# Performance work log

Measured on AMD Instinct MI355X. Metric: run time of the kernel, lower is better.

The kernel has to match this reference:

```python
import jax, jax.numpy as jnp
import numpy as np

N_HEADS = 4
N_GROUPS = 32
EPS = 1e-5


def setup_inputs() -> dict:
    key = jax.random.key(0)
    ks = jax.random.split(key, 6)
    c = 512
    x = jax.random.normal(ks[0], (4, c, 64, 64), dtype=jnp.float32)
    # conv1x1 weights ~ kaiming-ish scale
    s = 1.0 / np.sqrt(c)
    wq = jax.random.normal(ks[1], (c, c), dtype=jnp.float32) * s
    wk = jax.random.normal(ks[2], (c, c), dtype=jnp.float32) * s
    wv = jax.random.normal(ks[3], (c, c), dtype=jnp.float32) * s
    wp = jax.random.normal(ks[4], (c, c), dtype=jnp.float32) * s
    zeros = jnp.zeros((c,), dtype=jnp.float32)
    return {
        "x": x,
        "gn_w": jnp.ones((c,), dtype=jnp.float32), "gn_b": zeros,
        "wq": wq, "bq": zeros, "wk": wk, "bk": zeros,
        "wv": wv, "bv": zeros, "wp": wp, "bp": zeros,
    }


def _group_norm(x, w, b):
    bsz, c, h, wd = x.shape
    xg = x.reshape(bsz, N_GROUPS, c // N_GROUPS, h, wd)
    mean = xg.mean(axis=(2, 3, 4), keepdims=True)
    var = xg.var(axis=(2, 3, 4), keepdims=True)
    xg = (xg - mean) * jax.lax.rsqrt(var + EPS)
    x = xg.reshape(bsz, c, h, wd)
    return x * w[None, :, None, None] + b[None, :, None, None]


def _conv1x1(x, w, b):
    # x: (b,c,h,w), w: (out,in) -> (b,out,h,w)
    return jnp.einsum('bchw,oc->bohw', x, w) + b[None, :, None, None]


def reference(x, gn_w, gn_b, wq, bq, wk, bk, wv, bv, wp, bp):
    bsz, c, h, wd = x.shape
    hd = c // N_HEADS
    hw = h * wd
    x_n = _group_norm(x, gn_w, gn_b)
    q = _conv1x1(x_n, wq, bq)
    k = _conv1x1(x_n, wk, bk)
    v = _conv1x1(x_n, wv, bv)

    def to_heads(t):
        # (b,c,h,w) -> (b, n_heads, hw, head_dim)
        return t.reshape(bsz, N_HEADS, hd, hw).transpose(0, 1, 3, 2)

    q, k, v = to_heads(q), to_heads(k), to_heads(v)
    scale = hd ** (-0.5)
    attn = jnp.einsum('bhqd,bhkd->bhqk', q, k) * scale  # (b,H,hw,hw)
    attn = jax.nn.softmax(attn, axis=-1)
    out = jnp.einsum('bhqk,bhkd->bhqd', attn, v)
    out = out.transpose(0, 1, 3, 2).reshape(bsz, c, h, wd)
    out = _conv1x1(out, wp, bp)
    return x + out
```

## Files before the change

kernel.cpp:

```cpp
#include <hip/hip_runtime.h>
#include <math.h>

typedef __attribute__((ext_vector_type(8))) short short8;
typedef __attribute__((ext_vector_type(4))) float floatx4;
typedef __attribute__((ext_vector_type(16))) float floatx16;
typedef __attribute__((ext_vector_type(8))) unsigned short ushort8v;
typedef __attribute__((ext_vector_type(4))) unsigned short ushort4v;

#define HW 4096
#define CCH 512
#define NB 4
#define NH 4
#define HD 128

__device__ __forceinline__ unsigned short f2bf(float f) {
    union { float f; unsigned int u; } c; c.f = f;
    unsigned int u = c.u;
    u += 0x7FFFu + ((u >> 16) & 1u);
    return (unsigned short)(u >> 16);
}

__device__ __forceinline__ void gload_lds16(const unsigned short* g, unsigned short* l) {
    __builtin_amdgcn_global_load_lds(
        (const __attribute__((address_space(1))) unsigned int*)g,
        (__attribute__((address_space(3))) unsigned int*)l, 16, 0, 0);
}

__global__ void conv_w(const float* __restrict__ w0, const float* __restrict__ w1,
                       const float* __restrict__ w2, const float* __restrict__ w3,
                       unsigned short* __restrict__ dst) {
    const float* src = blockIdx.y == 0 ? w0 : blockIdx.y == 1 ? w1 : blockIdx.y == 2 ? w2 : w3;
    unsigned short* d = dst + (size_t)blockIdx.y * 262144;
    int i = blockIdx.x * 256 + threadIdx.x;
    float4 v = ((const float4*)src)[i];
    ushort4v o;
    o[0] = f2bf(v.x); o[1] = f2bf(v.y); o[2] = f2bf(v.z); o[3] = f2bf(v.w);
    ((ushort4v*)d)[i] = o;
}

__global__ void gn_stats(const float* __restrict__ x, float* __restrict__ stats) {
    int bg = blockIdx.x;
    int b = bg >> 5, g = bg & 31;
    const float4* p = (const float4*)(x + ((size_t)b * CCH + g * 16) * HW);
    float s = 0.f, ss = 0.f;
    for (int i = threadIdx.x; i < 16384; i += 256) {
        float4 v = p[i];
        s  += v.x + v.y + v.z + v.w;
        ss += v.x * v.x + v.y * v.y + v.z * v.z + v.w * v.w;
    }
    #pragma unroll
    for (int off = 32; off > 0; off >>= 1) {
        s  += __shfl_down(s, off, 64);
        ss += __shfl_down(ss, off, 64);
    }
    __shared__ float sm[4], sm2[4];
    int wid = threadIdx.x >> 6;
    if ((threadIdx.x & 63) == 0) { sm[wid] = s; sm2[wid] = ss; }
    __syncthreads();
    if (threadIdx.x == 0) {
        float ts = sm[0] + sm[1] + sm[2] + sm[3];
        float tss = sm2[0] + sm2[1] + sm2[2] + sm2[3];
        float mean = ts * (1.f / 65536.f);
        float var = tss * (1.f / 65536.f) - mean * mean;
        stats[bg * 2] = mean;
        stats[bg * 2 + 1] = rsqrtf(var + 1e-5f);
    }
}

__global__ void gn_apply(const float* __restrict__ x, const float* __restrict__ gnw,
                         const float* __restrict__ gnb, const float* __restrict__ stats,
                         unsigned short* __restrict__ xt) {
    int s = blockIdx.x * 256 + threadIdx.x;
    int g = blockIdx.y, b = blockIdx.z;
    float mean = stats[(b * 32 + g) * 2];
    float rstd = stats[(b * 32 + g) * 2 + 1];
    const float* xb = x + ((size_t)b * CCH + g * 16) * HW + s;
    unsigned short outv[16];
    #pragma unroll
    for (int cl = 0; cl < 16; cl++) {
        int c = g * 16 + cl;
        float v = xb[(size_t)cl * HW];
        v = (v - mean) * rstd * gnw[c] + gnb[c];
        outv[cl] = f2bf(v);
    }
    unsigned short* dst = xt + ((size_t)b * HW + s) * CCH + g * 16;
    *(ushort8v*)dst       = *(ushort8v*)&outv[0];
    *(ushort8v*)(dst + 8) = *(ushort8v*)&outv[8];
}

template <int MODE>
__global__ __launch_bounds__(256, 3) void gemm_nt(
    const unsigned short* __restrict__ A, long long aStride,
    const unsigned short* __restrict__ Bm, long long bStride,
    const float* __restrict__ bias, float scale,
    const float* __restrict__ resid, long long rStride,
    void* __restrict__ Cp, long long cStride, int ldc) {
    __shared__ __align__(16) unsigned short lA[128 * 64];
    __shared__ __align__(16) unsigned short lB[128 * 64];
    const int tid = threadIdx.x;
    const int lane = tid & 63;
    const int wid = tid >> 6;
    const int z = blockIdx.z;
    const unsigned short* Ab = A + (size_t)z * aStride + (size_t)blockIdx.x * 128 * 512;
    const unsigned short* Bb = Bm + (size_t)z * bStride + (size_t)blockIdx.y * 128 * 512;

    floatx4 acc[4][4];
    #pragma unroll
    for (int i = 0; i < 4; i++)
        #pragma unroll
        for (int j = 0; j < 4; j++) acc[i][j] = (floatx4)0.f;

    const int wm = (wid >> 1) * 64;
    const int wn = (wid & 1) * 64;
    const int l15 = lane & 15;
    const int l4 = lane >> 4;
    const int sxr = l15 & 7;

    size_t srcOff[4];
    int dstBase[4];
    #pragma unroll
    for (int n = 0; n < 4; n++) {
        int row = n * 32 + (tid >> 3);
        int g = tid & 7;
        srcOff[n] = (size_t)row * 512 + (size_t)((g ^ (row & 7)) << 3);
        dstBase[n] = (n * 256 + wid * 64) * 8;
    }

    #pragma unroll 1
    for (int t = 0; t < 8; t++) {
        int k0 = t * 64;
        #pragma unroll
        for (int n = 0; n < 4; n++) gload_lds16(&Ab[srcOff[n] + k0], lA + dstBase[n]);
        #pragma unroll
        for (int n = 0; n < 4; n++) gload_lds16(&Bb[srcOff[n] + k0], lB + dstBase[n]);
        __syncthreads();
        #pragma unroll
        for (int kk = 0; kk < 2; kk++) {
            short8 af[4], bf[4];
            #pragma unroll
            for (int i = 0; i < 4; i++)
                af[i] = *(const short8*)&lA[(wm + i * 16 + l15) * 64 + (((kk * 4 + l4) ^ sxr) << 3)];
            #pragma unroll
            for (int j = 0; j < 4; j++)
                bf[j] = *(const short8*)&lB[(wn + j * 16 + l15) * 64 + (((kk * 4 + l4) ^ sxr) << 3)];
            #pragma unroll
            for (int i = 0; i < 4; i++)
                #pragma unroll
                for (int j = 0; j < 4; j++)
                    acc[i][j] = __builtin_amdgcn_mfma_f32_16x16x32_bf16(af[i], bf[j], acc[i][j], 0, 0, 0);
        }
        if (t < 7) __syncthreads();
    }

    long long m0 = (long long)blockIdx.x * 128 + wm;
    long long n0 = (long long)blockIdx.y * 128 + wn;
    if (MODE == 3 && blockIdx.z == 1) {
        unsigned short* C = (unsigned short*)Cp + (size_t)cStride;
        #pragma unroll
        for (int i = 0; i < 4; i++)
            #pragma unroll
            for (int j = 0; j < 4; j++) {
                long long col = n0 + j * 16 + l15;
                float bv = resid[col];
                int hh = (int)(col >> 7);
                int d = (int)(col & 127);
                size_t dpart = (size_t)(d >> 3) * 512 + (size_t)(d & 7);
                #pragma unroll
                for (int r = 0; r < 4; r++) {
                    long long row = m0 + i * 16 + l4 * 4 + r;
                    int bb = (int)(row >> 12), s = (int)(row & 4095);
                    size_t addr = (size_t)(bb * NH + hh) * 524288
                                + (size_t)(s >> 6) * 8192 + dpart + (size_t)(s & 63) * 8;
                    C[addr] = f2bf(acc[i][j][r] + bv);
                }
            }
    } else if (MODE == 0 || MODE == 3) {
        unsigned short* C = (unsigned short*)Cp + (size_t)z * cStride;
        #pragma unroll
        for (int i = 0; i < 4; i++)
            #pragma unroll
            for (int j = 0; j < 4; j++) {
                long long col = n0 + j * 16 + l15;
                float bv = bias[col];
                #pragma unroll
                for (int r = 0; r < 4; r++) {
                    long long row = m0 + i * 16 + l4 * 4 + r;
                    C[row * ldc + col] = f2bf((acc[i][j][r] + bv) * scale);
                }
            }
    } else if (MODE == 1) {
        float* C = (float*)Cp + (size_t)z * cStride;
        const float* R = resid + (size_t)z * rStride;
        #pragma unroll
        for (int i = 0; i < 4; i++)
            #pragma unroll
            for (int j = 0; j < 4; j++)
                #pragma unroll
                for (int r = 0; r < 4; r++) {
                    long long row = m0 + i * 16 + l4 * 4 + r;
                    long long col = n0 + j * 16 + l15;
                    C[row * ldc + col] = acc[i][j][r] + bias[row] + R[row * ldc + col];
                }
    } else {
        unsigned short* C = (unsigned short*)Cp;
        const int b = z;
        #pragma unroll
        for (int i = 0; i < 4; i++)
            #pragma unroll
            for (int j = 0; j < 4; j++)
                #pragma unroll
                for (int r = 0; r < 4; r++) {
                    long long row = m0 + i * 16 + l4 * 4 + r;
                    long long col = n0 + j * 16 + l15;
                    int hh = (int)(row >> 7);
                    int d = (int)(row & 127);
                    int s = (int)col;
                    size_t addr = (size_t)(b * NH + hh) * 524288
                                + (size_t)(s >> 6) * 8192
                                + (size_t)(((s & 63) >> 3) * 128 + d) * 8 + (size_t)(s & 7);
                    C[addr] = f2bf(acc[i][j][r] + bias[row]);
                }
    }
}

__global__ __launch_bounds__(512, 2) void attn_kern(
    const unsigned short* __restrict__ Qb, const unsigned short* __restrict__ Kp,
    const unsigned short* __restrict__ Vp, unsigned short* __restrict__ Ob) {
    __shared__ __align__(16) unsigned short lk0[8192], lk1[8192];
    __shared__ __align__(16) unsigned short lv0[8192], lv1[8192];
    const int tid = threadIdx.x;
    const int lane = tid & 63;
    const int w = tid >> 6;
    const int l31 = lane & 31;
    const int l1 = lane >> 5;
    const int bid = blockIdx.x;
    const int g = bid & 15;
    const int qt = bid >> 4;
    const int h = g & 3, b = g >> 2;
    const int q0 = qt * 256;
    const size_t headOff = (size_t)h * HD;
    const size_t batchRow = (size_t)b * HW;
    const unsigned short* KpB = Kp + (size_t)(b * NH + h) * 524288;
    const unsigned short* VpB = Vp + (size_t)(b * NH + h) * 524288;

    const size_t dmaOff = (size_t)(w * 128 + lane) * 8;
    const int ldsOff = w * 1024;

    short8 qf[8];
    #pragma unroll
    for (int kd = 0; kd < 8; kd++)
        qf[kd] = *(const short8*)&Qb[(batchRow + q0 + w * 32 + l31) * 512
                                     + headOff + kd * 16 + l1 * 8];

    short8 onesf;
    #pragma unroll
    for (int e = 0; e < 8; e++) onesf[e] = (short)0x3F80;

    floatx16 acc_o[4];
    floatx16 acc_l;
    acc_l = (floatx16)0.f;
    #pragma unroll
    for (int dj = 0; dj < 4; dj++) acc_o[dj] = (floatx16)0.f;

    #pragma unroll
    for (int n = 0; n < 2; n++) gload_lds16(&KpB[dmaOff + n * 512], lk0 + ldsOff + n * 512);
    #pragma unroll
    for (int n = 0; n < 2; n++) gload_lds16(&KpB[dmaOff + 8192 + n * 512], lk1 + ldsOff + n * 512);
    #pragma unroll
    for (int n = 0; n < 2; n++) gload_lds16(&VpB[dmaOff + n * 512], lv0 + ldsOff + n * 512);
    __syncthreads();

    floatx16 sa0 = (floatx16)0.f, sa1 = (floatx16)0.f;
    #pragma unroll
    for (int kd = 0; kd < 8; kd++) {
        short8 kf0 = *(const short8*)&lk0[(kd * 2 + l1) * 512 + l31 * 8];
        short8 kf1 = *(const short8*)&lk0[(kd * 2 + l1) * 512 + 256 + l31 * 8];
        sa0 = __builtin_amdgcn_mfma_f32_32x32x16_bf16(kf0, qf[kd], sa0, 0, 0, 0);
        sa1 = __builtin_amdgcn_mfma_f32_32x32x16_bf16(kf1, qf[kd], sa1, 0, 0, 0);
    }
    __syncthreads();

    unsigned short* lvCur = lv0;  unsigned short* lvNxt = lv1;
    unsigned short* kRead = lk1;  unsigned short* kWrite = lk0;

    #pragma unroll 1
    for (int kt = 0; kt < 63; kt++) {
        {
            size_t tv = (size_t)(kt + 1) * 8192;
            size_t tk = (size_t)(kt + 2) * 8192;
            #pragma unroll
            for (int n = 0; n < 2; n++) gload_lds16(&VpB[dmaOff + tv + n * 512], lvNxt + ldsOff + n * 512);
            #pragma unroll
            for (int n = 0; n < 2; n++) gload_lds16(&KpB[dmaOff + tk + n * 512], kWrite + ldsOff + n * 512);
        }

        short8 paf[4];
        #pragma unroll
        for (int r = 0; r < 16; r++) sa0[r] = __builtin_amdgcn_exp2f(sa0[r]);
        #pragma unroll
        for (int r = 0; r < 16; r++) sa1[r] = __builtin_amdgcn_exp2f(sa1[r]);
        #pragma unroll
        for (int tb = 0; tb < 2; tb++) {
            const floatx16& sa = tb ? sa1 : sa0;
            unsigned int wv[4][2];
            #pragma unroll
            for (int gg = 0; gg < 4; gg++) {
                asm("v_cvt_pk_bf16_f32 %0, %1, %2" : "=v"(wv[gg][0])
                    : "v"(sa[4 * gg + 0]), "v"(sa[4 * gg + 1]));
                asm("v_cvt_pk_bf16_f32 %0, %1, %2" : "=v"(wv[gg][1])
                    : "v"(sa[4 * gg + 2]), "v"(sa[4 * gg + 3]));
            }
            #pragma unroll
            for (int hh = 0; hh < 2; hh++) {
                unsigned int a0 = wv[2 * hh][0], b0 = wv[2 * hh + 1][0];
                unsigned int a1 = wv[2 * hh][1], b1 = wv[2 * hh + 1][1];
                asm("v_permlane32_swap_b32 %0, %1" : "+v"(a0), "+v"(b0));
                asm("v_permlane32_swap_b32 %0, %1" : "+v"(a1), "+v"(b1));
                union { unsigned int u[4]; short8 s8; } f;
                f.u[0] = a0; f.u[1] = a1; f.u[2] = b0; f.u[3] = b1;
                paf[2 * tb + hh] = f.s8;
            }
        }

        sa0 = (floatx16)0.f; sa1 = (floatx16)0.f;
        __builtin_amdgcn_s_setprio(1);
        #pragma unroll
        for (int u = 0; u < 4; u++) {
            #pragma unroll
            for (int q2 = 0; q2 < 2; q2++) {
                int kd = u * 2 + q2;
                short8 kf0 = *(const short8*)&kRead[(kd * 2 + l1) * 512 + l31 * 8];
                short8 kf1 = *(const short8*)&kRead[(kd * 2 + l1) * 512 + 256 + l31 * 8];
                sa0 = __builtin_amdgcn_mfma_f32_32x32x16_bf16(kf0, qf[kd], sa0, 0, 0, 0);
                sa1 = __builtin_amdgcn_mfma_f32_32x32x16_bf16(kf1, qf[kd], sa1, 0, 0, 0);
            }
            acc_l = __builtin_amdgcn_mfma_f32_32x32x16_bf16(paf[u], onesf, acc_l, 0, 0, 0);
            #pragma unroll
            for (int dj = 0; dj < 4; dj++) {
                short8 vv = *(const short8*)&lvCur[(u * 2 + l1) * 1024 + dj * 256 + l31 * 8];
                acc_o[dj] = __builtin_amdgcn_mfma_f32_32x32x16_bf16(paf[u], vv, acc_o[dj], 0, 0, 0);
            }
        }
        __builtin_amdgcn_s_setprio(0);

        __syncthreads();
        unsigned short* t;
        t = lvCur; lvCur = lvNxt; lvNxt = t;
        t = kRead; kRead = kWrite; kWrite = t;
    }

    {
        short8 paf[4];
        #pragma unroll
        for (int r = 0; r < 16; r++) sa0[r] = __builtin_amdgcn_exp2f(sa0[r]);
        #pragma unroll
        for (int r = 0; r < 16; r++) sa1[r] = __builtin_amdgcn_exp2f(sa1[r]);
        #pragma unroll
        for (int tb = 0; tb < 2; tb++) {
            const floatx16& sa = tb ? sa1 : sa0;
            unsigned int wv[4][2];
            #pragma unroll
            for (int gg = 0; gg < 4; gg++) {
                asm("v_cvt_pk_bf16_f32 %0, %1, %2" : "=v"(wv[gg][0])
                    : "v"(sa[4 * gg + 0]), "v"(sa[4 * gg + 1]));
                asm("v_cvt_pk_bf16_f32 %0, %1, %2" : "=v"(wv[gg][1])
                    : "v"(sa[4 * gg + 2]), "v"(sa[4 * gg + 3]));
            }
            #pragma unroll
            for (int hh = 0; hh < 2; hh++) {
                unsigned int a0 = wv[2 * hh][0], b0 = wv[2 * hh + 1][0];
                unsigned int a1 = wv[2 * hh][1], b1 = wv[2 * hh + 1][1];
                asm("v_permlane32_swap_b32 %0, %1" : "+v"(a0), "+v"(b0));
                asm("v_permlane32_swap_b32 %0, %1" : "+v"(a1), "+v"(b1));
                union { unsigned int u[4]; short8 s8; } f;
                f.u[0] = a0; f.u[1] = a1; f.u[2] = b0; f.u[3] = b1;
                paf[2 * tb + hh] = f.s8;
            }
        }
        __builtin_amdgcn_s_setprio(1);
        #pragma unroll
        for (int u = 0; u < 4; u++) {
            acc_l = __builtin_amdgcn_mfma_f32_32x32x16_bf16(paf[u], onesf, acc_l, 0, 0, 0);
            #pragma unroll
            for (int dj = 0; dj < 4; dj++) {
                short8 vv = *(const short8*)&lvCur[(u * 2 + l1) * 1024 + dj * 256 + l31 * 8];
                acc_o[dj] = __builtin_amdgcn_mfma_f32_32x32x16_bf16(paf[u], vv, acc_o[dj], 0, 0, 0);
            }
        }
        __builtin_amdgcn_s_setprio(0);
    }

    #pragma unroll
    for (int gg = 0; gg < 4; gg++)
        #pragma unroll
        for (int p = 0; p < 4; p++) {
            int reg = 4 * gg + p;
            float rl = 1.f / acc_l[reg];
            int qr = p + 8 * gg + 4 * l1;
            size_t row = batchRow + q0 + w * 32 + qr;
            #pragma unroll
            for (int dj = 0; dj < 4; dj++)
                Ob[row * 512 + headOff + dj * 32 + l31] = f2bf(acc_o[dj][reg] * rl);
        }
}

extern "C" void kernel_launch(void* const* d_in, const int* in_sizes, int n_in,
                              void* d_out, int out_size, void* d_ws, size_t ws_size,
                              hipStream_t stream) {
    const float* x   = (const float*)d_in[0];
    const float* gnw = (const float*)d_in[1];
    const float* gnb = (const float*)d_in[2];
    const float* wq  = (const float*)d_in[3];
    const float* bq  = (const float*)d_in[4];
    const float* wk  = (const float*)d_in[5];
    const float* bk  = (const float*)d_in[6];
    const float* wv  = (const float*)d_in[7];
    const float* bv  = (const float*)d_in[8];
    const float* wp  = (const float*)d_in[9];
    const float* bp  = (const float*)d_in[10];
    float* out = (float*)d_out;

    const size_t NE = (size_t)NB * HW * CCH;
    unsigned short* ws16 = (unsigned short*)d_ws;
    unsigned short* XT = ws16;
    unsigned short* Qb = ws16 + NE;
    unsigned short* Kb = ws16 + 2 * NE;
    unsigned short* Vt = ws16 + 3 * NE;
    unsigned short* Wb = ws16 + 4 * NE;
    float* stats = (float*)(ws16 + 4 * NE + 4 * 262144);

    const float qscale = 0.08838834764831845f * 1.4426950408889634f;

    conv_w<<<dim3(256, 4), 256, 0, stream>>>(wq, wk, wv, wp, Wb);
    gn_stats<<<128, 256, 0, stream>>>(x, stats);
    gn_apply<<<dim3(16, 32, 4), 256, 0, stream>>>(x, gnw, gnb, stats, XT);

    gemm_nt<3><<<dim3(128, 4, 2), 256, 0, stream>>>(XT, 0, Wb, 262144, bq, qscale, bk, 0,
                                                    Qb, (long long)NE, 512);
    gemm_nt<2><<<dim3(4, 32, 4), 256, 0, stream>>>(Wb + 2 * 262144, 0, XT, (long long)HW * 512, bv, 1.f,
                                                   nullptr, 0, Vt, 0, HW);

    unsigned short* Ob = XT;
    attn_kern<<<dim3(256), dim3(512), 0, stream>>>(Qb, Kb, Vt, Ob);

    gemm_nt<1><<<dim3(4, 32, 4), 256, 0, stream>>>(Wb + 3 * 262144, 0, Ob, (long long)HW * 512, bp, 1.f,
                                                   x, (long long)CCH * HW, out, (long long)CCH * HW, HW);
}
```

Measured before the change: 322.0 us.

## Replace ones-MFMA row sum with VALU reduction and unroll attention loop by two

The softmax denominator was accumulated by an extra MFMA against a vector of ones. It is now summed in fp32 on the VALU per lane, then combined across half-waves with a permlane swap and a shuffle at the end. The key loop is unrolled by two with ping-pong score accumulators, so the next tile's QK MFMAs are issued before the current tile's exp, pack and PV. This is meant to cut MFMA work and let the exp/convert VALU work overlap the MFMAs, at the cost of more registers. The row sum now uses fp32 values rather than bf16-rounded ones, which changes rounding slightly.

Result: no change. 319.8 us (-0.7%).

```diff
diff --git a/kernel.cpp b/kernel.cpp
--- a/kernel.cpp
+++ b/kernel.cpp
@@ -24,6 +24,11 @@
     __builtin_amdgcn_global_load_lds(
         (const __attribute__((address_space(1))) unsigned int*)g,
         (__attribute__((address_space(3))) unsigned int*)l, 16, 0, 0);
+}
+
+__device__ __forceinline__ float sum16(const floatx16& s) {
+    return ((((s[0] + s[1]) + (s[2] + s[3])) + ((s[4] + s[5]) + (s[6] + s[7])))
+          + (((s[8] + s[9]) + (s[10] + s[11])) + ((s[12] + s[13]) + (s[14] + s[15]))));
 }
 
 __global__ void conv_w(const float* __restrict__ w0, const float* __restrict__ w1,
@@ -252,15 +257,10 @@
         qf[kd] = *(const short8*)&Qb[(batchRow + q0 + w * 32 + l31) * 512
                                      + headOff + kd * 16 + l1 * 8];
 
-    short8 onesf;
-    #pragma unroll
-    for (int e = 0; e < 8; e++) onesf[e] = (short)0x3F80;
-
     floatx16 acc_o[4];
-    floatx16 acc_l;
-    acc_l = (floatx16)0.f;
     #pragma unroll
     for (int dj = 0; dj < 4; dj++) acc_o[dj] = (floatx16)0.f;
+    float lsum_part = 0.f;
 
     #pragma unroll
     for (int n = 0; n < 2; n++) gload_lds16(&KpB[dmaOff + n * 512], lk0 + ldsOff + n * 512);
@@ -270,124 +270,102 @@
     for (int n = 0; n < 2; n++) gload_lds16(&VpB[dmaOff + n * 512], lv0 + ldsOff + n * 512);
     __syncthreads();
 
-    floatx16 sa0 = (floatx16)0.f, sa1 = (floatx16)0.f;
+    floatx16 saA0 = (floatx16)0.f, saA1 = (floatx16)0.f;
+    floatx16 saB0, saB1;
     #pragma unroll
     for (int kd = 0; kd < 8; kd++) {
         short8 kf0 = *(const short8*)&lk0[(kd * 2 + l1) * 512 + l31 * 8];
         short8 kf1 = *(const short8*)&lk0[(kd * 2 + l1) * 512 + 256 + l31 * 8];
-        sa0 = __builtin_amdgcn_mfma_f32_32x32x16_bf16(kf0, qf[kd], sa0, 0, 0, 0);
-        sa1 = __builtin_amdgcn_mfma_f32_32x32x16_bf16(kf1, qf[kd], sa1, 0, 0, 0);
+        saA0 = __builtin_amdgcn_mfma_f32_32x32x16_bf16(kf0, qf[kd], saA0, 0, 0, 0);
+        saA1 = __builtin_amdgcn_mfma_f32_32x32x16_bf16(kf1, qf[kd], saA1, 0, 0, 0);
     }
     __syncthreads();
 
     unsigned short* lvCur = lv0;  unsigned short* lvNxt = lv1;
     unsigned short* kRead = lk1;  unsigned short* kWrite = lk0;
 
+#define ATTN_PACK(S0, S1)                                                                 \
+    short8 paf[4];                                                                        \
+    {                                                                                     \
+        _Pragma("unroll") for (int r = 0; r < 16; r++) S0[r] = __builtin_amdgcn_exp2f(S0[r]); \
+        _Pragma("unroll") for (int r = 0; r < 16; r++) S1[r] = __builtin_amdgcn_exp2f(S1[r]); \
+        lsum_part += sum16(S0) + sum16(S1);                                               \
+        _Pragma("unroll") for (int tb = 0; tb < 2; tb++) {                                \
+            const floatx16& sa_ = tb ? S1 : S0;                                           \
+            unsigned int wv[4][2];                                                        \
+            _Pragma("unroll") for (int gg = 0; gg < 4; gg++) {                            \
+                asm("v_cvt_pk_bf16_f32 %0, %1, %2" : "=v"(wv[gg][0])                      \
+                    : "v"(sa_[4 * gg + 0]), "v"(sa_[4 * gg + 1]));                        \
+                asm("v_cvt_pk_bf16_f32 %0, %1, %2" : "=v"(wv[gg][1])                      \
+                    : "v"(sa_[4 * gg + 2]), "v"(sa_[4 * gg + 3]));                        \
+            }                                                                             \
+            _Pragma("unroll") for (int hh = 0; hh < 2; hh++) {                            \
+                unsigned int a0 = wv[2 * hh][0], b0 = wv[2 * hh + 1][0];                  \
+                unsigned int a1 = wv[2 * hh][1], b1 = wv[2 * hh + 1][1];                  \
+                asm("v_permlane32_swap_b32 %0, %1" : "+v"(a0), "+v"(b0));                 \
+                asm("v_permlane32_swap_b32 %0, %1" : "+v"(a1), "+v"(b1));                 \
+                union { unsigned int u[4]; short8 s8; } f_;                               \
+                f_.u[0] = a0; f_.u[1] = a1; f_.u[2] = b0; f_.u[3] = b1;                   \
+                paf[2 * tb + hh] = f_.s8;                                                 \
+            }                                                                             \
+        }                                                                                 \
+    }
+
+#define ATTN_PV                                                                           \
+    _Pragma("unroll") for (int u = 0; u < 4; u++) {                                       \
+        _Pragma("unroll") for (int dj = 0; dj < 4; dj++) {                                \
+            short8 vv = *(const short8*)&lvCur[(u * 2 + l1) * 1024 + dj * 256 + l31 * 8]; \
+            acc_o[dj] = __builtin_amdgcn_mfma_f32_32x32x16_bf16(paf[u], vv, acc_o[dj], 0, 0, 0); \
+        }                                                                                 \
+    }
+
+#define ATTN_STEP(KT, SO0, SO1, SN0, SN1)                                                 \
+    {                                                                                     \
+        size_t tv = (size_t)((KT) + 1) * 8192;                                            \
+        size_t tk = (size_t)((KT) + 2) * 8192;                                            \
+        _Pragma("unroll") for (int n = 0; n < 2; n++)                                     \
+            gload_lds16(&VpB[dmaOff + tv + n * 512], lvNxt + ldsOff + n * 512);           \
+        _Pragma("unroll") for (int n = 0; n < 2; n++)                                     \
+            gload_lds16(&KpB[dmaOff + tk + n * 512], kWrite + ldsOff + n * 512);          \
+        SN0 = (floatx16)0.f; SN1 = (floatx16)0.f;                                         \
+        __builtin_amdgcn_s_setprio(1);                                                    \
+        _Pragma("unroll") for (int kd = 0; kd < 8; kd++) {                                \
+            short8 kf0 = *(const short8*)&kRead[(kd * 2 + l1) * 512 + l31 * 8];           \
+            short8 kf1 = *(const short8*)&kRead[(kd * 2 + l1) * 512 + 256 + l31 * 8];     \
+            SN0 = __builtin_amdgcn_mfma_f32_32x32x16_bf16(kf0, qf[kd], SN0, 0, 0, 0);     \
+            SN1 = __builtin_amdgcn_mfma_f32_32x32x16_bf16(kf1, qf[kd], SN1, 0, 0, 0);     \
+        }                                                                                 \
+        ATTN_PACK(SO0, SO1)                                                               \
+        ATTN_PV                                                                           \
+        __builtin_amdgcn_s_setprio(0);                                                    \
+        __syncthreads();                                                                  \
+        { unsigned short* t_ = lvCur; lvCur = lvNxt; lvNxt = t_;                          \
+          t_ = kRead; kRead = kWrite; kWrite = t_; }                                      \
+    }
+
     #pragma unroll 1
-    for (int kt = 0; kt < 63; kt++) {
-        {
-            size_t tv = (size_t)(kt + 1) * 8192;
-            size_t tk = (size_t)(kt + 2) * 8192;
-            #pragma unroll
-            for (int n = 0; n < 2; n++) gload_lds16(&VpB[dmaOff + tv + n * 512], lvNxt + ldsOff + n * 512);
-            #pragma unroll
-            for (int n = 0; n < 2; n++) gload_lds16(&KpB[dmaOff + tk + n * 512], kWrite + ldsOff + n * 512);
-        }
-
-        short8 paf[4];
-        #pragma unroll
-        for (int r = 0; r < 16; r++) sa0[r] = __builtin_amdgcn_exp2f(sa0[r]);
-        #pragma unroll
-        for (int r = 0; r < 16; r++) sa1[r] = __builtin_amdgcn_exp2f(sa1[r]);
-        #pragma unroll
-        for (int tb = 0; tb < 2; tb++) {
-            const floatx16& sa = tb ? sa1 : sa0;
-            unsigned int wv[4][2];
-            #pragma unroll
-            for (int gg = 0; gg < 4; gg++) {
-                asm("v_cvt_pk_bf16_f32 %0, %1, %2" : "=v"(wv[gg][0])
-                    : "v"(sa[4 * gg + 0]), "v"(sa[4 * gg + 1]));
-                asm("v_cvt_pk_bf16_f32 %0, %1, %2" : "=v"(wv[gg][1])
-                    : "v"(sa[4 * gg + 2]), "v"(sa[4 * gg + 3]));
-            }
-            #pragma unroll
-            for (int hh = 0; hh < 2; hh++) {
-                unsigned int a0 = wv[2 * hh][0], b0 = wv[2 * hh + 1][0];
-                unsigned int a1 = wv[2 * hh][1], b1 = wv[2 * hh + 1][1];
-                asm("v_permlane32_swap_b32 %0, %1" : "+v"(a0), "+v"(b0));
-                asm("v_permlane32_swap_b32 %0, %1" : "+v"(a1), "+v"(b1));
-                union { unsigned int u[4]; short8 s8; } f;
-                f.u[0] = a0; f.u[1] = a1; f.u[2] = b0; f.u[3] = b1;
-                paf[2 * tb + hh] = f.s8;
-            }
-        }
-
-        sa0 = (floatx16)0.f; sa1 = (floatx16)0.f;
+    for (int it = 0; it < 31; it++) {
+        ATTN_STEP(2 * it,     saA0, saA1, saB0, saB1);
+        ATTN_STEP(2 * it + 1, saB0, saB1, saA0, saA1);
+    }
+    ATTN_STEP(62, saA0, saA1, saB0, saB1);
+
+    {
+        ATTN_PACK(saB0, saB1)
         __builtin_amdgcn_s_setprio(1);
-        #pragma unroll
-        for (int u = 0; u < 4; u++) {
-            #pragma unroll
-            for (int q2 = 0; q2 < 2; q2++) {
-                int kd = u * 2 + q2;
-                short8 kf0 = *(const short8*)&kRead[(kd * 2 + l1) * 512 + l31 * 8];
-                short8 kf1 = *(const short8*)&kRead[(kd * 2 + l1) * 512 + 256 + l31 * 8];
-                sa0 = __builtin_amdgcn_mfma_f32_32x32x16_bf16(kf0, qf[kd], sa0, 0, 0, 0);
-                sa1 = __builtin_amdgcn_mfma_f32_32x32x16_bf16(kf1, qf[kd], sa1, 0, 0, 0);
-            }
-            acc_l = __builtin_amdgcn_mfma_f32_32x32x16_bf16(paf[u], onesf, acc_l, 0, 0, 0);
-            #pragma unroll
-            for (int dj = 0; dj < 4; dj++) {
-                short8 vv = *(const short8*)&lvCur[(u * 2 + l1) * 1024 + dj * 256 + l31 * 8];
-                acc_o[dj] = __builtin_amdgcn_mfma_f32_32x32x16_bf16(paf[u], vv, acc_o[dj], 0, 0, 0);
-            }
-        }
+        ATTN_PV
         __builtin_amdgcn_s_setprio(0);
-
-        __syncthreads();
-        unsigned short* t;
-        t = lvCur; lvCur = lvNxt; lvNxt = t;
-        t = kRead; kRead = kWrite; kWrite = t;
-    }
-
+    }
+#undef ATTN_STEP
+#undef ATTN_PV
+#undef ATTN_PACK
+
+    float tot;
     {
-        short8 paf[4];
-        #pragma unroll
-        for (int r = 0; r < 16; r++) sa0[r] = __builtin_amdgcn_exp2f(sa0[r]);
-        #pragma unroll
-        for (int r = 0; r < 16; r++) sa1[r] = __builtin_amdgcn_exp2f(sa1[r]);
-        #pragma unroll
-        for (int tb = 0; tb < 2; tb++) {
-            const floatx16& sa = tb ? sa1 : sa0;
-            unsigned int wv[4][2];
-            #pragma unroll
-            for (int gg = 0; gg < 4; gg++) {
-                asm("v_cvt_pk_bf16_f32 %0, %1, %2" : "=v"(wv[gg][0])
-                    : "v"(sa[4 * gg + 0]), "v"(sa[4 * gg + 1]));
-                asm("v_cvt_pk_bf16_f32 %0, %1, %2" : "=v"(wv[gg][1])
-                    : "v"(sa[4 * gg + 2]), "v"(sa[4 * gg + 3]));
-            }
-            #pragma unroll
-            for (int hh = 0; hh < 2; hh++) {
-                unsigned int a0 = wv[2 * hh][0], b0 = wv[2 * hh + 1][0];
-                unsigned int a1 = wv[2 * hh][1], b1 = wv[2 * hh + 1][1];
-                asm("v_permlane32_swap_b32 %0, %1" : "+v"(a0), "+v"(b0));
-                asm("v_permlane32_swap_b32 %0, %1" : "+v"(a1), "+v"(b1));
-                union { unsigned int u[4]; short8 s8; } f;
-                f.u[0] = a0; f.u[1] = a1; f.u[2] = b0; f.u[3] = b1;
-                paf[2 * tb + hh] = f.s8;
-            }
-        }
-        __builtin_amdgcn_s_setprio(1);
-        #pragma unroll
-        for (int u = 0; u < 4; u++) {
-            acc_l = __builtin_amdgcn_mfma_f32_32x32x16_bf16(paf[u], onesf, acc_l, 0, 0, 0);
-            #pragma unroll
-            for (int dj = 0; dj < 4; dj++) {
-                short8 vv = *(const short8*)&lvCur[(u * 2 + l1) * 1024 + dj * 256 + l31 * 8];
-                acc_o[dj] = __builtin_amdgcn_mfma_f32_32x32x16_bf16(paf[u], vv, acc_o[dj], 0, 0, 0);
-            }
-        }
-        __builtin_amdgcn_s_setprio(0);
+        union { float f; unsigned int u; } ua, ub;
+        ua.f = lsum_part; ub.f = lsum_part;
+        asm("v_permlane32_swap_b32 %0, %1" : "+v"(ua.u), "+v"(ub.u));
+        tot = ua.f + ub.f;
     }
 
     #pragma unroll
@@ -395,8 +373,8 @@
         #pragma unroll
         for (int p = 0; p < 4; p++) {
             int reg = 4 * gg + p;
-            float rl = 1.f / acc_l[reg];
             int qr = p + 8 * gg + 4 * l1;
+            float rl = 1.f / __shfl(tot, qr, 64);
             size_t row = batchRow + q0 + w * 32 + qr;
             #pragma unroll
             for (int dj = 0; dj < 4; dj++)
```
